# Kernel optimization log

Hardware: AMD Instinct MI355X
Metric: run time of the kernel (lower is better)

Reference implementation:

```python
import jax, jax.numpy as jnp
import numpy as np

COMMITMENT_LOSS_WEIGHT = 0.25


def setup_inputs() -> dict:
    key = jax.random.key(0)
    k1, k2 = jax.random.split(key)
    B, H, W, C = 64, 32, 32, 256
    D, K = H * W, 1024  # embedding_dim = H*W per the rearrange+reshape in call()
    x = jax.random.normal(k1, (B, H, W, C), dtype=jnp.float32)
    # Orthogonal initializer (like tf.keras.initializers.Orthogonal) via QR
    E = jnp.linalg.qr(jax.random.normal(k2, (D, K), dtype=jnp.float32))[0]
    return {"x": x, "embeddings": E.astype(jnp.float32)}


def reference(x, embeddings):
    B, H, W, C = x.shape
    D = H * W  # embedding_dim
    # einops: 'b h w c -> b c (h w)'
    cont = jnp.transpose(x, (0, 3, 1, 2)).reshape(B, C, D)
    flat = cont.reshape(-1, D)  # [B*C, D]
    # squared L2 distances via norm + matmul (as in get_discretised)
    dists = (jnp.sum(flat * flat, axis=1, keepdims=True)
             + jnp.sum(embeddings * embeddings, axis=0)
             - 2.0 * (flat @ embeddings))  # [B*C, K]
    idx = jnp.argmin(dists, axis=1)  # [B*C]
    # one_hot @ embeddings.T == direct gather of codebook columns
    quantised = embeddings.T[idx].reshape(B, C, D)
    codebook_loss = jnp.mean((jax.lax.stop_gradient(cont) - quantised) ** 2)
    commitment_loss = COMMITMENT_LOSS_WEIGHT * jnp.mean(
        (cont - jax.lax.stop_gradient(quantised)) ** 2)
    loss = codebook_loss + commitment_loss  # layer add_loss terms, summed
    # einops: 'b c (h w) -> b h w c'
    q_bhwc = jnp.transpose(quantised.reshape(B, C, H, W), (0, 2, 3, 1))
    discretised = idx.reshape(-1, C)  # [B, C]
    # straight-through estimator
    q_out = x + jax.lax.stop_gradient(q_bhwc - x)
    return q_out, discretised, loss
```

## Files before the change

### kernel.cpp

```cpp
#include <hip/hip_runtime.h>
#include <float.h>
#include <stdint.h>

#define B_   64
#define C_   256
#define D_   1024
#define K_   1024
#define M_   16384
#define NX_  16777216
#define DISC_OFF NX_
#define LOSS_OFF (NX_ + M_)

typedef _Float16 h8 __attribute__((ext_vector_type(8)));
typedef float    f4 __attribute__((ext_vector_type(4)));

#define XSCALE 512.0f
#define ESCALE 2048.0f
#define DOT_UNSCALE_2 (2.0f / 1048576.0f)

#define WS_EH  0
#define WS_EL  524288
#define WS_CN  1048576
#define WS_PCN 1049600
#define WS_PV  1180672
#define WS_PI  1311744


__device__ __forceinline__ void async16(const _Float16* g, _Float16* l) {
    __builtin_amdgcn_global_load_lds(
        (const __attribute__((address_space(1))) unsigned int*)g,
        (__attribute__((address_space(3))) unsigned int*)l, 16, 0, 0);
}

__global__ __launch_bounds__(256) void esplit_kernel(const float* __restrict__ E,
                                                     _Float16* __restrict__ Eh,
                                                     _Float16* __restrict__ El,
                                                     float* __restrict__ pcn) {
    const int tid = blockIdx.x * 256 + threadIdx.x;
    const int n   = tid & 1023;
    const int o   = tid >> 10;
    const int d0  = o * 8;
    h8 hh, ll;
    float s = 0.f;
    #pragma unroll
    for (int i = 0; i < 8; ++i) {
        const float v = E[(size_t)(d0 + i) * K_ + n];
        s = fmaf(v, v, s);
        const float vs = v * ESCALE;
        const _Float16 h = (_Float16)vs;
        hh[i] = h;
        ll[i] = (_Float16)(vs - (float)h);
    }
    pcn[o * K_ + n] = s;
    const int nt   = n >> 4;
    const int kt   = o >> 2;
    const int lane = (n & 15) + (o & 3) * 16;
    const size_t off = ((size_t)(nt * 32 + kt) * 64 + lane) * 8;
    *(h8*)(Eh + off) = hh;
    *(h8*)(El + off) = ll;
}

__global__ __launch_bounds__(256) void colnorm2_kernel(const float* __restrict__ pcn,
                                                       float* __restrict__ cn,
                                                       float* __restrict__ loss_slot) {
    const int k = blockIdx.x * 256 + threadIdx.x;
    float s = 0.f;
    for (int i = 0; i < 128; ++i) s += pcn[i * K_ + k];
    cn[k] = s;
    if (k == 0) *loss_slot = 0.0f;
}

__global__ __launch_bounds__(256) void xsplit_kernel(const float* __restrict__ x,
                                                     _Float16* __restrict__ Xh,
                                                     _Float16* __restrict__ Xl) {
    const int tid = blockIdx.x * 256 + threadIdx.x;
    const int m   = tid & 16383;
    const int o   = tid >> 14;
    const int b   = m >> 8, c = m & 255;
    const int d0  = o * 8;
    const float* xp = x + ((size_t)(b * 1024 + d0) * 256) + c;
    h8 hh, ll;
    #pragma unroll
    for (int i = 0; i < 8; ++i) {
        const float v  = xp[(size_t)i * 256];
        const float vs = v * XSCALE;
        const _Float16 h = (_Float16)vs;
        hh[i] = h;
        ll[i] = (_Float16)(vs - (float)h);
    }
    const int mt   = m >> 4;
    const int kt   = o >> 2;
    const int lane = (m & 15) + (o & 3) * 16;
    const size_t off = ((size_t)(mt * 32 + kt) * 64 + lane) * 8;
    *(h8*)(Xh + off) = hh;
    *(h8*)(Xl + off) = ll;
}

__global__ __launch_bounds__(256, 3) void gemm_argmin_kernel(
        const _Float16* __restrict__ Xh, const _Float16* __restrict__ Xl,
        const _Float16* __restrict__ Eh, const _Float16* __restrict__ El,
        const float* __restrict__ cn,
        float* __restrict__ pV, int* __restrict__ pI) {
    __shared__ _Float16 Abuf[16 * 512];
    __shared__ _Float16 Bbuf[16 * 512];
    __shared__ float cV[128][2];
    __shared__ int   cI[128][2];

    const int t    = threadIdx.x;
    const int rt   = blockIdx.x >> 3;
    const int ct   = blockIdx.x & 7;
    const int wave = t >> 6, lane = t & 63;
    const int lo16 = lane & 15, hi4 = lane >> 4;
    const int mq   = (wave & 1) * 64;
    const int nq   = (wave >> 1) * 64;
    const int mt0  = rt * 8, nt0 = ct * 8;
    const int n0g  = ct * 128;

    const _Float16* gsrc[8];
    _Float16*       ldst[8];
    #pragma unroll
    for (int i = 0; i < 8; ++i) {
        const int id  = wave * 8 + i;
        const int p   = (id >> 3) & 1;
        const int tix = id & 7;
        if (id < 16) {
            const _Float16* base = p ? Xl : Xh;
            gsrc[i] = base + ((size_t)(mt0 + tix) * 32) * 512 + lane * 8;
            ldst[i] = &Abuf[(p * 8 + tix) * 512];
        } else {
            const _Float16* base = p ? El : Eh;
            gsrc[i] = base + ((size_t)(nt0 + tix) * 32) * 512 + lane * 8;
            ldst[i] = &Bbuf[(p * 8 + tix) * 512];
        }
    }

    f4 acc[4][4];
    const f4 zero = {0.f, 0.f, 0.f, 0.f};
    #pragma unroll
    for (int i = 0; i < 4; ++i)
        #pragma unroll
        for (int j = 0; j < 4; ++j) acc[i][j] = zero;

    for (int ks = 0; ks < 32; ++ks) {
        __syncthreads();
        #pragma unroll
        for (int i = 0; i < 8; ++i)
            async16(gsrc[i] + ks * 512, ldst[i]);
        __syncthreads();

        h8 Bf[2][4];
        #pragma unroll
        for (int tn = 0; tn < 4; ++tn) {
            const int tixn = (nq >> 4) + tn;
            Bf[0][tn] = *(const h8*)&Bbuf[tixn * 512 + lane * 8];
            Bf[1][tn] = *(const h8*)&Bbuf[(8 + tixn) * 512 + lane * 8];
        }
        #pragma unroll
        for (int tm = 0; tm < 4; ++tm) {
            const int tixm = (mq >> 4) + tm;
            const h8 Ah = *(const h8*)&Abuf[tixm * 512 + lane * 8];
            const h8 Al = *(const h8*)&Abuf[(8 + tixm) * 512 + lane * 8];
            #pragma unroll
            for (int tn = 0; tn < 4; ++tn) {
                acc[tm][tn] = __builtin_amdgcn_mfma_f32_16x16x32_f16(Ah, Bf[0][tn], acc[tm][tn], 0, 0, 0);
                acc[tm][tn] = __builtin_amdgcn_mfma_f32_16x16x32_f16(Ah, Bf[1][tn], acc[tm][tn], 0, 0, 0);
                acc[tm][tn] = __builtin_amdgcn_mfma_f32_16x16x32_f16(Al, Bf[0][tn], acc[tm][tn], 0, 0, 0);
            }
        }
    }

    float cnv[4];
    #pragma unroll
    for (int tn = 0; tn < 4; ++tn) cnv[tn] = cn[n0g + nq + tn * 16 + lo16];

    #pragma unroll
    for (int tm = 0; tm < 4; ++tm) {
        #pragma unroll
        for (int r = 0; r < 4; ++r) {
            float bv = FLT_MAX;
            int   bi = 0;
            #pragma unroll
            for (int tn = 0; tn < 4; ++tn) {
                const float v = cnv[tn] - acc[tm][tn][r] * DOT_UNSCALE_2;
                if (v < bv) { bv = v; bi = nq + tn * 16 + lo16; }
            }
            #pragma unroll
            for (int msk = 1; msk < 16; msk <<= 1) {
                const float ov = __shfl_xor(bv, msk, 64);
                const int   oi = __shfl_xor(bi, msk, 64);
                if (ov < bv || (ov == bv && oi < bi)) { bv = ov; bi = oi; }
            }
            if (lo16 == 0) {
                const int row = mq + tm * 16 + hi4 * 4 + r;
                cV[row][wave >> 1] = bv;
                cI[row][wave >> 1] = bi;
            }
        }
    }
    __syncthreads();
    if (t < 128) {
        const float v0 = cV[t][0], v1 = cV[t][1];
        const int   i0 = cI[t][0], i1 = cI[t][1];
        float bv; int bi;
        if (v1 < v0) { bv = v1; bi = i1; } else { bv = v0; bi = i0; }
        const int row = rt * 128 + t;
        pV[row * 8 + ct] = bv;
        pI[row * 8 + ct] = n0g + bi;
    }
}

__global__ __launch_bounds__(256) void reduce_kernel(const float* __restrict__ pV,
                                                     const int* __restrict__ pI,
                                                     float* __restrict__ disc) {
    const int rid = blockIdx.x * 256 + threadIdx.x;
    float bv = FLT_MAX;
    int   bi = 0;
    #pragma unroll
    for (int c = 0; c < 8; ++c) {
        const float v = pV[rid * 8 + c];
        const int   i = pI[rid * 8 + c];
        if (v < bv || (v == bv && i < bi)) { bv = v; bi = i; }
    }
    disc[rid] = (float)bi;
}

__global__ __launch_bounds__(256) void finalize_kernel(const float* __restrict__ x,
                                                       const float* __restrict__ E,
                                                       const float* __restrict__ discf,
                                                       float* __restrict__ out,
                                                       float* __restrict__ loss) {
    __shared__ float Erow[1024];
    const int t = threadIdx.x;
    const int d = blockIdx.x;
    *(float4*)&Erow[t * 4] = *(const float4*)(E + (size_t)d * K_ + t * 4);
    __syncthreads();

    const int bl = t >> 6;
    const int c4 = (t & 63) * 4;
    float lsum = 0.f;
    #pragma unroll 4
    for (int bg = 0; bg < 64; bg += 4) {
        const int b = bg + bl;
        const float4 id4 = *(const float4*)(discf + b * 256 + c4);
        const size_t xoff = ((size_t)(b * 1024 + d) << 8) + c4;
        const float4 xv = *(const float4*)(x + xoff);
        const float e0 = Erow[(int)id4.x];
        const float e1 = Erow[(int)id4.y];
        const float e2 = Erow[(int)id4.z];
        const float e3 = Erow[(int)id4.w];
        float4 qv;
        qv.x = xv.x + (e0 - xv.x);
        qv.y = xv.y + (e1 - xv.y);
        qv.z = xv.z + (e2 - xv.z);
        qv.w = xv.w + (e3 - xv.w);
        *(float4*)(out + xoff) = qv;
        const float d0 = xv.x - e0, d1 = xv.y - e1, d2 = xv.z - e2, d3 = xv.w - e3;
        lsum += fmaf(d0, d0, fmaf(d1, d1, fmaf(d2, d2, d3 * d3)));
    }

    #pragma unroll
    for (int off = 32; off > 0; off >>= 1)
        lsum += __shfl_down(lsum, off);
    __shared__ float wsum[4];
    if ((t & 63) == 0) wsum[t >> 6] = lsum;
    __syncthreads();
    if (t == 0) {
        const float s = (wsum[0] + wsum[1]) + (wsum[2] + wsum[3]);
        atomicAdd(loss, s * (1.25f / 16777216.0f));
    }
}

extern "C" void kernel_launch(void* const* d_in, const int* in_sizes, int n_in,
                              void* d_out, int out_size, void* d_ws, size_t ws_size,
                              hipStream_t stream) {
    (void)in_sizes; (void)n_in; (void)out_size; (void)ws_size;
    const float* x = (const float*)d_in[0];
    const float* E = (const float*)d_in[1];
    float* out = (float*)d_out;
    float* ws  = (float*)d_ws;

    _Float16* Eh = (_Float16*)(ws + WS_EH);
    _Float16* El = (_Float16*)(ws + WS_EL);
    float* cn    = ws + WS_CN;
    float* pcn   = ws + WS_PCN;
    float* pV    = ws + WS_PV;
    int*   pI    = (int*)(ws + WS_PI);

    _Float16* Xh = (_Float16*)out;
    _Float16* Xl = (_Float16*)out + NX_;
    float* disc  = out + DISC_OFF;
    float* loss  = out + LOSS_OFF;

    esplit_kernel  <<<512,  256, 0, stream>>>(E, Eh, El, pcn);
    colnorm2_kernel<<<4,    256, 0, stream>>>(pcn, cn, loss);
    xsplit_kernel  <<<8192, 256, 0, stream>>>(x, Xh, Xl);
    gemm_argmin_kernel<<<1024, 256, 0, stream>>>(Xh, Xl, Eh, El, cn, pV, pI);
    reduce_kernel  <<<64,   256, 0, stream>>>(pV, pI, disc);
    finalize_kernel<<<1024, 256, 0, stream>>>(x, E, disc, out, loss);
}
```

Measured before the change: 274.4 us.

## Double-buffer GEMM LDS tiles, widen N tile to 256, merge split kernels

```diff
diff --git a/kernel.cpp b/kernel.cpp
--- a/kernel.cpp
+++ b/kernel.cpp
@@ -23,8 +23,7 @@
 #define WS_CN  1048576
 #define WS_PCN 1049600
 #define WS_PV  1180672
-#define WS_PI  1311744
-
+#define WS_PI  1246208
 
 __device__ __forceinline__ void async16(const _Float16* g, _Float16* l) {
     __builtin_amdgcn_global_load_lds(
@@ -32,32 +31,60 @@
         (__attribute__((address_space(3))) unsigned int*)l, 16, 0, 0);
 }
 
-__global__ __launch_bounds__(256) void esplit_kernel(const float* __restrict__ E,
-                                                     _Float16* __restrict__ Eh,
-                                                     _Float16* __restrict__ El,
-                                                     float* __restrict__ pcn) {
-    const int tid = blockIdx.x * 256 + threadIdx.x;
-    const int n   = tid & 1023;
-    const int o   = tid >> 10;
-    const int d0  = o * 8;
-    h8 hh, ll;
-    float s = 0.f;
-    #pragma unroll
-    for (int i = 0; i < 8; ++i) {
-        const float v = E[(size_t)(d0 + i) * K_ + n];
-        s = fmaf(v, v, s);
-        const float vs = v * ESCALE;
-        const _Float16 h = (_Float16)vs;
-        hh[i] = h;
-        ll[i] = (_Float16)(vs - (float)h);
-    }
-    pcn[o * K_ + n] = s;
-    const int nt   = n >> 4;
-    const int kt   = o >> 2;
-    const int lane = (n & 15) + (o & 3) * 16;
-    const size_t off = ((size_t)(nt * 32 + kt) * 64 + lane) * 8;
-    *(h8*)(Eh + off) = hh;
-    *(h8*)(El + off) = ll;
+__global__ __launch_bounds__(256) void split_kernel(const float* __restrict__ x,
+                                                    const float* __restrict__ E,
+                                                    _Float16* __restrict__ Xh,
+                                                    _Float16* __restrict__ Xl,
+                                                    _Float16* __restrict__ Eh,
+                                                    _Float16* __restrict__ El,
+                                                    float* __restrict__ pcn) {
+    const int bid = blockIdx.x;
+    if (bid < 512) {
+        const int tid = bid * 256 + threadIdx.x;
+        const int n   = tid & 1023;
+        const int o   = tid >> 10;
+        const int d0  = o * 8;
+        h8 hh, ll;
+        float s = 0.f;
+        #pragma unroll
+        for (int i = 0; i < 8; ++i) {
+            const float v = E[(size_t)(d0 + i) * K_ + n];
+            s = fmaf(v, v, s);
+            const float vs = v * ESCALE;
+            const _Float16 h = (_Float16)vs;
+            hh[i] = h;
+            ll[i] = (_Float16)(vs - (float)h);
+        }
+        pcn[o * K_ + n] = s;
+        const int nt   = n >> 4;
+        const int kt   = o >> 2;
+        const int lane = (n & 15) + (o & 3) * 16;
+        const size_t off = ((size_t)(nt * 32 + kt) * 64 + lane) * 8;
+        *(h8*)(Eh + off) = hh;
+        *(h8*)(El + off) = ll;
+    } else {
+        const int tid = (bid - 512) * 256 + threadIdx.x;
+        const int m   = tid & 16383;
+        const int o   = tid >> 14;
+        const int b   = m >> 8, c = m & 255;
+        const int d0  = o * 8;
+        const float* xp = x + ((size_t)(b * 1024 + d0) * 256) + c;
+        h8 hh, ll;
+        #pragma unroll
+        for (int i = 0; i < 8; ++i) {
+            const float v  = xp[(size_t)i * 256];
+            const float vs = v * XSCALE;
+            const _Float16 h = (_Float16)vs;
+            hh[i] = h;
+            ll[i] = (_Float16)(vs - (float)h);
+        }
+        const int mt   = m >> 4;
+        const int kt   = o >> 2;
+        const int lane = (m & 15) + (o & 3) * 16;
+        const size_t off = ((size_t)(mt * 32 + kt) * 64 + lane) * 8;
+        *(h8*)(Xh + off) = hh;
+        *(h8*)(Xl + off) = ll;
+    }
 }
 
 __global__ __launch_bounds__(256) void colnorm2_kernel(const float* __restrict__ pcn,
@@ -70,67 +97,46 @@
     if (k == 0) *loss_slot = 0.0f;
 }
 
-__global__ __launch_bounds__(256) void xsplit_kernel(const float* __restrict__ x,
-                                                     _Float16* __restrict__ Xh,
-                                                     _Float16* __restrict__ Xl) {
-    const int tid = blockIdx.x * 256 + threadIdx.x;
-    const int m   = tid & 16383;
-    const int o   = tid >> 14;
-    const int b   = m >> 8, c = m & 255;
-    const int d0  = o * 8;
-    const float* xp = x + ((size_t)(b * 1024 + d0) * 256) + c;
-    h8 hh, ll;
-    #pragma unroll
-    for (int i = 0; i < 8; ++i) {
-        const float v  = xp[(size_t)i * 256];
-        const float vs = v * XSCALE;
-        const _Float16 h = (_Float16)vs;
-        hh[i] = h;
-        ll[i] = (_Float16)(vs - (float)h);
-    }
-    const int mt   = m >> 4;
-    const int kt   = o >> 2;
-    const int lane = (m & 15) + (o & 3) * 16;
-    const size_t off = ((size_t)(mt * 32 + kt) * 64 + lane) * 8;
-    *(h8*)(Xh + off) = hh;
-    *(h8*)(Xl + off) = ll;
-}
-
-__global__ __launch_bounds__(256, 3) void gemm_argmin_kernel(
+__global__ __launch_bounds__(512, 2) void gemm_argmin_kernel(
         const _Float16* __restrict__ Xh, const _Float16* __restrict__ Xl,
         const _Float16* __restrict__ Eh, const _Float16* __restrict__ El,
         const float* __restrict__ cn,
         float* __restrict__ pV, int* __restrict__ pI) {
-    __shared__ _Float16 Abuf[16 * 512];
-    __shared__ _Float16 Bbuf[16 * 512];
-    __shared__ float cV[128][2];
-    __shared__ int   cI[128][2];
+    extern __shared__ _Float16 smem[];
+    _Float16* Ab0 = smem;
+    _Float16* Ab1 = smem + 8192;
+    _Float16* Bb0 = smem + 16384;
+    _Float16* Bb1 = smem + 32768;
+    float* cV = (float*)(smem + 49152);
+    int*   cI = (int*)(cV + 512);
 
     const int t    = threadIdx.x;
-    const int rt   = blockIdx.x >> 3;
-    const int ct   = blockIdx.x & 7;
+    const int rt   = blockIdx.x >> 2;
+    const int ct   = blockIdx.x & 3;
     const int wave = t >> 6, lane = t & 63;
     const int lo16 = lane & 15, hi4 = lane >> 4;
     const int mq   = (wave & 1) * 64;
     const int nq   = (wave >> 1) * 64;
-    const int mt0  = rt * 8, nt0 = ct * 8;
-    const int n0g  = ct * 128;
-
-    const _Float16* gsrc[8];
-    _Float16*       ldst[8];
-    #pragma unroll
-    for (int i = 0; i < 8; ++i) {
-        const int id  = wave * 8 + i;
-        const int p   = (id >> 3) & 1;
-        const int tix = id & 7;
+    const int mt0  = rt * 8, nt0 = ct * 16;
+    const int n0g  = ct * 256;
+
+    const _Float16* src[6];
+    _Float16* dst0[6];
+    _Float16* dst1[6];
+    #pragma unroll
+    for (int i = 0; i < 6; ++i) {
+        const int id = wave * 6 + i;
         if (id < 16) {
-            const _Float16* base = p ? Xl : Xh;
-            gsrc[i] = base + ((size_t)(mt0 + tix) * 32) * 512 + lane * 8;
-            ldst[i] = &Abuf[(p * 8 + tix) * 512];
+            const int plane = id >> 3, mt = id & 7;
+            src[i]  = (plane ? Xl : Xh) + ((size_t)(mt0 + mt) * 32) * 512 + lane * 8;
+            dst0[i] = Ab0 + (plane * 8 + mt) * 512 + lane * 8;
+            dst1[i] = Ab1 + (plane * 8 + mt) * 512 + lane * 8;
         } else {
-            const _Float16* base = p ? El : Eh;
-            gsrc[i] = base + ((size_t)(nt0 + tix) * 32) * 512 + lane * 8;
-            ldst[i] = &Bbuf[(p * 8 + tix) * 512];
+            const int q = id - 16;
+            const int plane = q >> 4, nt = q & 15;
+            src[i]  = (plane ? El : Eh) + ((size_t)(nt0 + nt) * 32) * 512 + lane * 8;
+            dst0[i] = Bb0 + (plane * 16 + nt) * 512 + lane * 8;
+            dst1[i] = Bb1 + (plane * 16 + nt) * 512 + lane * 8;
         }
     }
 
@@ -141,19 +147,26 @@
         #pragma unroll
         for (int j = 0; j < 4; ++j) acc[i][j] = zero;
 
-    for (int ks = 0; ks < 32; ++ks) {
+    #pragma unroll
+    for (int i = 0; i < 6; ++i) async16(src[i], dst0[i]);
+
+    for (int s = 0; s < 32; ++s) {
+        const int cur = s & 1;
         __syncthreads();
-        #pragma unroll
-        for (int i = 0; i < 8; ++i)
-            async16(gsrc[i] + ks * 512, ldst[i]);
-        __syncthreads();
+        if (s + 1 < 32) {
+            #pragma unroll
+            for (int i = 0; i < 6; ++i)
+                async16(src[i] + (size_t)(s + 1) * 512, cur ? dst0[i] : dst1[i]);
+        }
+        const _Float16* Abuf = cur ? Ab1 : Ab0;
+        const _Float16* Bbuf = cur ? Bb1 : Bb0;
 
         h8 Bf[2][4];
         #pragma unroll
         for (int tn = 0; tn < 4; ++tn) {
             const int tixn = (nq >> 4) + tn;
             Bf[0][tn] = *(const h8*)&Bbuf[tixn * 512 + lane * 8];
-            Bf[1][tn] = *(const h8*)&Bbuf[(8 + tixn) * 512 + lane * 8];
+            Bf[1][tn] = *(const h8*)&Bbuf[(16 + tixn) * 512 + lane * 8];
         }
         #pragma unroll
         for (int tm = 0; tm < 4; ++tm) {
@@ -192,20 +205,25 @@
             }
             if (lo16 == 0) {
                 const int row = mq + tm * 16 + hi4 * 4 + r;
-                cV[row][wave >> 1] = bv;
-                cI[row][wave >> 1] = bi;
+                const int g   = wave >> 1;
+                cV[row * 4 + g] = bv;
+                cI[row * 4 + g] = bi;
             }
         }
     }
     __syncthreads();
     if (t < 128) {
-        const float v0 = cV[t][0], v1 = cV[t][1];
-        const int   i0 = cI[t][0], i1 = cI[t][1];
-        float bv; int bi;
-        if (v1 < v0) { bv = v1; bi = i1; } else { bv = v0; bi = i0; }
+        float bv = FLT_MAX;
+        int   bi = 0;
+        #pragma unroll
+        for (int g = 0; g < 4; ++g) {
+            const float v = cV[t * 4 + g];
+            const int   i = cI[t * 4 + g];
+            if (v < bv || (v == bv && i < bi)) { bv = v; bi = i; }
+        }
         const int row = rt * 128 + t;
-        pV[row * 8 + ct] = bv;
-        pI[row * 8 + ct] = n0g + bi;
+        pV[row * 4 + ct] = bv;
+        pI[row * 4 + ct] = n0g + bi;
     }
 }
 
@@ -216,9 +234,9 @@
     float bv = FLT_MAX;
     int   bi = 0;
     #pragma unroll
-    for (int c = 0; c < 8; ++c) {
-        const float v = pV[rid * 8 + c];
-        const int   i = pI[rid * 8 + c];
+    for (int c = 0; c < 4; ++c) {
+        const float v = pV[rid * 4 + c];
+        const int   i = pI[rid * 4 + c];
         if (v < bv || (v == bv && i < bi)) { bv = v; bi = i; }
     }
     disc[rid] = (float)bi;
@@ -291,10 +309,14 @@
     float* disc  = out + DISC_OFF;
     float* loss  = out + LOSS_OFF;
 
-    esplit_kernel  <<<512,  256, 0, stream>>>(E, Eh, El, pcn);
+    static bool attr_set = false;
+    hipFuncSetAttribute((const void*)gemm_argmin_kernel,
+                        hipFuncAttributeMaxDynamicSharedMemorySize, 102400);
+    (void)attr_set;
+
+    split_kernel   <<<8704, 256, 0, stream>>>(x, E, Xh, Xl, Eh, El, pcn);
     colnorm2_kernel<<<4,    256, 0, stream>>>(pcn, cn, loss);
-    xsplit_kernel  <<<8192, 256, 0, stream>>>(x, Xh, Xl);
-    gemm_argmin_kernel<<<1024, 256, 0, stream>>>(Xh, Xl, Eh, El, cn, pV, pI);
+    gemm_argmin_kernel<<<512, 512, 102400, stream>>>(Xh, Xl, Eh, El, cn, pV, pI);
     reduce_kernel  <<<64,   256, 0, stream>>>(pV, pI, disc);
     finalize_kernel<<<1024, 256, 0, stream>>>(x, E, disc, out, loss);
 }
```

New measurement: 249.2 us. -9.2%, faster.
